# Kernel tuning notes

Measured on AMD Instinct MI355X. Metric: run time of the kernel, lower is better.

Reference implementation:

```python
import jax, jax.numpy as jnp
import numpy as np

N = 50000      # nodes
E = 800000     # edges (avg degree 16)
DIM = 256      # in_channels == heads * out_channels
H = 8          # heads
C = DIM // H   # per-head out_channels = 32
EDGE_DIM = 2
NEG_SLOPE = 0.2


def setup_inputs() -> dict:
    key = jax.random.key(0)
    ks = jax.random.split(key, 8)
    x = jax.random.normal(ks[0], (N, DIM), dtype=jnp.float32)
    edge_index = jax.random.randint(ks[1], (2, E), 0, N, dtype=jnp.int32)
    edge_attr = jax.random.normal(ks[2], (E, EDGE_DIM), dtype=jnp.float32)
    s = 1.0 / np.sqrt(DIM)
    W_l = jax.random.normal(ks[3], (DIM, H * C), dtype=jnp.float32) * s   # lin_l (src)
    W_r = jax.random.normal(ks[4], (DIM, H * C), dtype=jnp.float32) * s   # lin_r (dst)
    W_e = jax.random.normal(ks[5], (EDGE_DIM, H * C), dtype=jnp.float32) * (1.0 / np.sqrt(EDGE_DIM))
    att = jax.random.normal(ks[6], (H, C), dtype=jnp.float32) * s         # attention vector a
    bias = jnp.zeros((H * C,), dtype=jnp.float32)
    return {"x": x, "edge_index": edge_index, "edge_attr": edge_attr,
            "W_l": W_l, "W_r": W_r, "W_e": W_e, "att": att, "bias": bias}


def reference(x, edge_index, edge_attr, W_l, W_r, W_e, att, bias):
    src, dst = edge_index[0], edge_index[1]
    # --- add self loops; fill_value='mean' => scatter-mean of incoming edge_attr per node ---
    attr_sum = jax.ops.segment_sum(edge_attr, dst, num_segments=N)          # [N, 2]
    cnt = jax.ops.segment_sum(jnp.ones((edge_attr.shape[0], 1), edge_attr.dtype), dst, num_segments=N)
    loop_attr = attr_sum / jnp.maximum(cnt, 1.0)                             # [N, 2], 0 for isolated nodes
    idx = jnp.arange(N, dtype=src.dtype)
    src_a = jnp.concatenate([src, idx])                                      # [E+N]
    dst_a = jnp.concatenate([dst, idx])
    ea = jnp.concatenate([edge_attr, loop_attr], axis=0)                     # [E+N, 2]
    # --- GATv2: project src/dst/edge features ---
    x_l = (x @ W_l).reshape(N, H, C)
    x_r = (x @ W_r).reshape(N, H, C)
    e_e = (ea @ W_e).reshape(-1, H, C)                                       # [E+N, H, C]
    m = x_l[src_a] + x_r[dst_a] + e_e                                        # [E+N, H, C]
    score = jnp.einsum('ehc,hc->eh', jax.nn.leaky_relu(m, NEG_SLOPE), att)   # [E+N, H]
    # --- segment softmax over incoming edges of each dst (self loop guarantees >=1 edge) ---
    smax = jax.ops.segment_max(score, dst_a, num_segments=N)                 # [N, H]
    ex = jnp.exp(score - smax[dst_a])
    denom = jax.ops.segment_sum(ex, dst_a, num_segments=N)                   # [N, H]
    alpha = ex / denom[dst_a]                                                # [E+N, H]
    # --- weighted scatter-add of src messages ---
    out = jax.ops.segment_sum(alpha[..., None] * x_l[src_a], dst_a, num_segments=N)  # [N, H, C]
    return out.reshape(N, H * C) + bias
```

## Files before the change

kernel.cpp:

```cpp
#include <hip/hip_runtime.h>
#include <hip/hip_bf16.h>

#define NN 50000
#define NPAD 53248
#define EE 800000
#define DIM 256
#define NEG_SLOPE 0.2f
#define LOG2E 1.44269504088896f

#define GEMM_BLOCKS 1564
#define FILL_BLOCKS 3125
#define CNT_BLOCKS  3125
#define CVT_BLOCKS  12500
#define WT_BLOCKS   512

typedef __attribute__((ext_vector_type(8))) short short8;
typedef __attribute__((ext_vector_type(4))) float f32x4;
typedef __attribute__((ext_vector_type(2))) float v2f;

__device__ __forceinline__ unsigned short f2bf(float f) {
    unsigned u = __float_as_uint(f);
    unsigned r = (u + 0x7fffu + ((u >> 16) & 1u)) >> 16;
    return (unsigned short)r;
}
__device__ __forceinline__ float bf2f(unsigned short h) {
    return __uint_as_float(((unsigned)h) << 16);
}
__device__ __forceinline__ float u2f_lo(unsigned u) {
    return __uint_as_float(u << 16);
}
__device__ __forceinline__ float u2f_hi(unsigned u) {
    return __uint_as_float(u & 0xffff0000u);
}

__device__ __forceinline__ float red8(float s) {
    int t;
    t = __builtin_amdgcn_update_dpp(0, __float_as_int(s), 0xB1, 0xF, 0xF, true);
    s += __int_as_float(t);
    t = __builtin_amdgcn_update_dpp(0, __float_as_int(s), 0x4E, 0xF, 0xF, true);
    s += __int_as_float(t);
    t = __builtin_amdgcn_update_dpp(0, __float_as_int(s), 0x141, 0xF, 0xF, true);
    s += __int_as_float(t);
    return s;
}

__global__ __launch_bounds__(256) void k_prep_count(
    const float* __restrict__ x, const float* __restrict__ Wl,
    const float* __restrict__ Wr, const int* __restrict__ ei,
    unsigned short* __restrict__ xb, unsigned short* __restrict__ wt,
    int* __restrict__ cnt, int* __restrict__ rank)
{
    int b = blockIdx.x;
    if (b < CNT_BLOCKS) {
        int e = b * 256 + threadIdx.x;
        if (e < EE) {
            int dst = ei[EE + e];
            rank[e] = atomicAdd(&cnt[dst], 1);
        }
    } else if (b < CNT_BLOCKS + CVT_BLOCKS) {
        int i = ((b - CNT_BLOCKS) * 256 + threadIdx.x) * 4;
        float4 v = *(const float4*)(x + i);
        ushort4 o;
        o.x = f2bf(v.x); o.y = f2bf(v.y); o.z = f2bf(v.z); o.w = f2bf(v.w);
        *(ushort4*)(xb + i) = o;
    } else {
        int idx = (b - CNT_BLOCKS - CVT_BLOCKS) * 256 + threadIdx.x;
        int n = idx >> 8, k = idx & 255;
        float v = (n < 256) ? Wl[k * 256 + n] : Wr[k * 256 + (n - 256)];
        wt[idx] = f2bf(v);
    }
}

__global__ __launch_bounds__(1024) void k_scan(
    const int* __restrict__ cnt, int* __restrict__ row_start)
{
    __shared__ int wsum[16];
    int tid = threadIdx.x, lane = tid & 63, wid = tid >> 6;
    int4 v[13];
#pragma unroll
    for (int p = 0; p < 13; ++p)
        v[p] = *(const int4*)(cnt + p * 4096 + tid * 4);
    int carry = 0;
#pragma unroll
    for (int p = 0; p < 13; ++p) {
        int4 vv = v[p];
        int tsum = vv.x + vv.y + vv.z + vv.w;
        int s = tsum;
#pragma unroll
        for (int off = 1; off < 64; off <<= 1) {
            int t = __shfl_up(s, off, 64);
            if (lane >= off) s += t;
        }
        if (lane == 63) wsum[wid] = s;
        __syncthreads();
        int wpre = 0, tot = 0;
#pragma unroll
        for (int w = 0; w < 16; ++w) {
            int xv = wsum[w];
            tot += xv;
            if (w < wid) wpre += xv;
        }
        int ex = carry + wpre + (s - tsum);
        int4 o;
        o.x = ex;
        o.y = o.x + vv.x;
        o.z = o.y + vv.y;
        o.w = o.z + vv.z;
        *(int4*)(row_start + p * 4096 + tid * 4) = o;
        carry += tot;
        __syncthreads();
    }
}

__global__ __launch_bounds__(256) void k_gemm_fill(
    const unsigned short* __restrict__ xb, const unsigned short* __restrict__ wt,
    const int* __restrict__ ei, const float* __restrict__ ea,
    const int* __restrict__ row_start, const int* __restrict__ rank,
    unsigned short* __restrict__ xl, unsigned short* __restrict__ xr,
    uint2* __restrict__ edge_rec)
{
    __shared__ short sAB[8192];
    int tid = threadIdx.x;

    if (blockIdx.x >= GEMM_BLOCKS) {
        int e = (blockIdx.x - GEMM_BLOCKS) * 256 + tid;
        if (e < EE) {
            int src = ei[e];
            int dst = ei[EE + e];
            float2 a = *(const float2*)(ea + 2 * e);
            int pos = row_start[dst] + rank[e];
            unsigned packed = ((unsigned)f2bf(a.y) << 16) | f2bf(a.x);
            edge_rec[pos] = make_uint2((unsigned)src, packed);
        }
        return;
    }

    int bid = blockIdx.x;
    const int q = GEMM_BLOCKS / 8, r = GEMM_BLOCKS % 8;
    int xcd = bid & 7, kk = bid >> 3;
    int wg = (xcd < r) ? xcd * (q + 1) + kk
                       : r * (q + 1) + (xcd - r) * q + kk;

    int wid = tid >> 6, lane = tid & 63;
    int mt = wg >> 2, nt = wg & 3;
    int mBase = mt * 128, nBase = nt * 128;
    int wm = (wid & 1) * 64, wn = (wid >> 1) * 64;
    int qq4 = lane >> 4, mh = lane & 15;

    f32x4 acc[4][4];
#pragma unroll
    for (int i = 0; i < 4; ++i)
#pragma unroll
        for (int j = 0; j < 4; ++j)
            acc[i][j] = (f32x4){0.f, 0.f, 0.f, 0.f};

    int aoff[4], boff[4];
#pragma unroll
    for (int f = 0; f < 4; ++f) {
        int rr = wm + f * 16 + mh;
        aoff[f] = (rr * 4 + (qq4 ^ (rr & 3))) * 8;
        int nl = wn + f * 16 + mh;
        boff[f] = 4096 + (nl * 4 + (qq4 ^ (nl & 3))) * 8;
    }

    for (int k0 = 0; k0 < 256; k0 += 32) {
        __syncthreads();
#pragma unroll
        for (int it = 0; it < 4; ++it) {
            int L = it * 256 + tid;
            const unsigned short* g;
            if (L < 512) {
                int rr = L >> 2;
                int q2 = (L & 3) ^ (rr & 3);
                int grow = mBase + rr;
                if (grow > NN - 1) grow = NN - 1;
                g = xb + (size_t)grow * 256 + k0 + q2 * 8;
            } else {
                int LB = L - 512;
                int nl = LB >> 2;
                int q2 = (LB & 3) ^ (nl & 3);
                g = wt + (size_t)(nBase + nl) * 256 + k0 + q2 * 8;
            }
            short* lp = sAB + (it * 256 + wid * 64) * 8;
            __builtin_amdgcn_global_load_lds(
                (const __attribute__((address_space(1))) void*)g,
                (__attribute__((address_space(3))) void*)lp, 16, 0, 0);
        }
        __syncthreads();

        short8 af[4], bfr[4];
#pragma unroll
        for (int f = 0; f < 4; ++f) af[f]  = *(const short8*)(sAB + aoff[f]);
#pragma unroll
        for (int f = 0; f < 4; ++f) bfr[f] = *(const short8*)(sAB + boff[f]);
#pragma unroll
        for (int i = 0; i < 4; ++i)
#pragma unroll
            for (int j = 0; j < 4; ++j)
                acc[i][j] = __builtin_amdgcn_mfma_f32_16x16x32_bf16(
                    af[i], bfr[j], acc[i][j], 0, 0, 0);
    }

    unsigned short* cb = (nt < 2) ? xl : xr;
    int chalf = (nt & 1) * 128;
#pragma unroll
    for (int i = 0; i < 4; ++i)
#pragma unroll
        for (int j = 0; j < 4; ++j)
#pragma unroll
            for (int rr = 0; rr < 4; ++rr) {
                int row = mBase + wm + i * 16 + qq4 * 4 + rr;
                if (row < NN) {
                    int col = chalf + wn + j * 16 + mh;
                    cb[(size_t)row * 256 + col] = f2bf(acc[i][j][rr]);
                }
            }
}

__global__ __launch_bounds__(256) void k_attn(
    const unsigned short* __restrict__ xl, const unsigned short* __restrict__ xr,
    const int* __restrict__ row_start, const uint2* __restrict__ edge_rec,
    const float* __restrict__ W_e, const float* __restrict__ att,
    const float* __restrict__ bias, float* __restrict__ out)
{
    int n = __builtin_amdgcn_readfirstlane(blockIdx.x * 4 + (threadIdx.x >> 6));
    if (n >= NN) return;
    int lane = threadIdx.x & 63;
    int j = lane * 4;

    uint2 xru = *(const uint2*)(xr + ((size_t)n << 8) + j);
    v2f xr01 = {u2f_lo(xru.x), u2f_hi(xru.x)};
    v2f xr23 = {u2f_lo(xru.y), u2f_hi(xru.y)};
    float4 av = *(const float4*)(att + j);
    v2f att01 = {av.x * LOG2E, av.y * LOG2E};
    v2f att23 = {av.z * LOG2E, av.w * LOG2E};
    float4 w0v = *(const float4*)(W_e + j);
    float4 w1v = *(const float4*)(W_e + 256 + j);
    v2f we0_01 = {w0v.x, w0v.y}, we0_23 = {w0v.z, w0v.w};
    v2f we1_01 = {w1v.x, w1v.y}, we1_23 = {w1v.z, w1v.w};
    const v2f sl2 = {NEG_SLOPE, NEG_SLOPE};

    int rs = __builtin_amdgcn_readfirstlane(row_start[n]);
    int cn = __builtin_amdgcn_readfirstlane(row_start[n + 1]) - rs;

    float D = 0.0f, la0 = 0.0f, la1 = 0.0f;
    v2f acc01 = {0.f, 0.f}, acc23 = {0.f, 0.f};

    auto body = [&](uint2 ru, float a0, float a1) {
        v2f xl01 = {u2f_lo(ru.x), u2f_hi(ru.x)};
        v2f xl23 = {u2f_lo(ru.y), u2f_hi(ru.y)};
        v2f a0v = {a0, a0}, a1v = {a1, a1};
        v2f m01 = xl01 + xr01;
        v2f m23 = xl23 + xr23;
        m01 = __builtin_elementwise_fma(a0v, we0_01, m01);
        m23 = __builtin_elementwise_fma(a0v, we0_23, m23);
        m01 = __builtin_elementwise_fma(a1v, we1_01, m01);
        m23 = __builtin_elementwise_fma(a1v, we1_23, m23);
        v2f t01 = __builtin_elementwise_max(m01, m01 * sl2);
        v2f t23 = __builtin_elementwise_max(m23, m23 * sl2);
        v2f sv = t01 * att01;
        sv = __builtin_elementwise_fma(t23, att23, sv);
        float s = sv.x + sv.y;
        s = red8(s);
        float w = __builtin_amdgcn_exp2f(s);
        D += w;
        v2f wv = {w, w};
        acc01 = __builtin_elementwise_fma(wv, xl01, acc01);
        acc23 = __builtin_elementwise_fma(wv, xl23, acc23);
    };

    int done = 0;
    while (done < cn) {
        int m = cn - done; if (m > 64) m = 64;
        int ridx = rs + done + lane;
        if (ridx > EE + 63) ridx = EE + 63;
        uint2 rc = edge_rec[ridx];
        int rcx = (int)rc.x, rca = (int)rc.y;

        auto gat = [&](int k) -> uint2 {
            unsigned sidx = (unsigned)__builtin_amdgcn_readlane(rcx, k);
            return *(const uint2*)(xl + ((size_t)sidx << 8) + j);
        };
        auto proc = [&](uint2 xu, int k) {
            unsigned pk = (unsigned)__builtin_amdgcn_readlane(rca, k);
            float a0 = __uint_as_float(pk << 16);
            float a1 = __uint_as_float(pk & 0xffff0000u);
            la0 += a0; la1 += a1;
            body(xu, a0, a1);
        };

        uint2 x0 = gat(0), x1 = gat(1), x2 = gat(2), x3 = gat(3);
        for (int i = 0; i < m; i += 4) {
            proc(x0, i);
            if (i + 4 < m) x0 = gat(i + 4);
            if (i + 1 < m) { proc(x1, i + 1); if (i + 5 < m) x1 = gat(i + 5); }
            if (i + 2 < m) { proc(x2, i + 2); if (i + 6 < m) x2 = gat(i + 6); }
            if (i + 3 < m) { proc(x3, i + 3); if (i + 7 < m) x3 = gat(i + 7); }
        }
        done += m;
    }

    float invc = 1.0f / fmaxf((float)cn, 1.0f);
    uint2 xs = *(const uint2*)(xl + ((size_t)n << 8) + j);
    body(xs, la0 * invc, la1 * invc);

    float invD = 1.0f / D;
    float4 b4 = *(const float4*)(bias + j);
    float4 o;
    o.x = fmaf(acc01.x, invD, b4.x);
    o.y = fmaf(acc01.y, invD, b4.y);
    o.z = fmaf(acc23.x, invD, b4.z);
    o.w = fmaf(acc23.y, invD, b4.w);
    *(float4*)(out + (size_t)n * 256 + j) = o;
}

extern "C" void kernel_launch(void* const* d_in, const int* in_sizes, int n_in,
                              void* d_out, int out_size, void* d_ws, size_t ws_size,
                              hipStream_t stream)
{
    const float* x    = (const float*)d_in[0];
    const int*   ei   = (const int*)  d_in[1];
    const float* ea   = (const float*)d_in[2];
    const float* Wl   = (const float*)d_in[3];
    const float* Wr   = (const float*)d_in[4];
    const float* We   = (const float*)d_in[5];
    const float* att  = (const float*)d_in[6];
    const float* bias = (const float*)d_in[7];
    float* out = (float*)d_out;

    char* ws = (char*)d_ws;
    size_t off = 0;
    unsigned short* xl = (unsigned short*)(ws + off); off += (size_t)NN * 256 * 2;
    unsigned short* xr = (unsigned short*)(ws + off); off += (size_t)NN * 256 * 2;
    unsigned short* xb = (unsigned short*)(ws + off); off += (size_t)NN * 256 * 2;
    uint2*  edge_rec   = (uint2*)(ws + off);          off += (size_t)(EE + 64) * 8;
    int*    cnt        = (int*)(ws + off);            off += (size_t)NPAD * 4;
    int*    row_st     = (int*)(ws + off);            off += (size_t)NPAD * 4;
    int*    rank       = (int*)(ws + off);            off += (size_t)EE * 4;
    unsigned short* wt = (unsigned short*)(ws + off); off += (size_t)512 * 256 * 2;

    hipMemsetAsync(edge_rec + EE, 0, 64 * sizeof(uint2) + NPAD * sizeof(int), stream);

    k_prep_count<<<CNT_BLOCKS + CVT_BLOCKS + WT_BLOCKS, 256, 0, stream>>>(
        x, Wl, Wr, ei, xb, wt, cnt, rank);
    k_scan      <<<1, 1024, 0, stream>>>(cnt, row_st);
    k_gemm_fill <<<GEMM_BLOCKS + FILL_BLOCKS, 256, 0, stream>>>(
        xb, wt, ei, ea, row_st, rank, xl, xr, edge_rec);
    k_attn      <<<12500, 256, 0, stream>>>(
        xl, xr, row_st, edge_rec, We, att, bias, out);
}
```

Before: 268.9 us.

## Split edge counting across prep and GEMM kernels, stage GEMM output via LDS

Edge degree counting is split in half: the first half runs in the prep kernel and the second half runs as extra blocks inside the GEMM kernel. The scan and the CSR fill then move after the GEMM into separate kernels, so the GEMM is no longer waiting on the serial single-block scan. The GEMM epilogue now stages its bf16 tile through padded LDS and writes it with coalesced 16-byte stores instead of scattered 2-byte stores. This adds one kernel launch and a serialized fill kernel.

```diff
diff --git a/kernel.cpp b/kernel.cpp
--- a/kernel.cpp
+++ b/kernel.cpp
@@ -4,13 +4,15 @@
 #define NN 50000
 #define NPAD 53248
 #define EE 800000
+#define EHALF 400128
 #define DIM 256
 #define NEG_SLOPE 0.2f
 #define LOG2E 1.44269504088896f
 
 #define GEMM_BLOCKS 1564
+#define CNTA_BLOCKS 1563
+#define CNTB_BLOCKS 1562
 #define FILL_BLOCKS 3125
-#define CNT_BLOCKS  3125
 #define CVT_BLOCKS  12500
 #define WT_BLOCKS   512
 
@@ -22,9 +24,6 @@
     unsigned u = __float_as_uint(f);
     unsigned r = (u + 0x7fffu + ((u >> 16) & 1u)) >> 16;
     return (unsigned short)r;
-}
-__device__ __forceinline__ float bf2f(unsigned short h) {
-    return __uint_as_float(((unsigned)h) << 16);
 }
 __device__ __forceinline__ float u2f_lo(unsigned u) {
     return __uint_as_float(u << 16);
@@ -44,94 +43,43 @@
     return s;
 }
 
-__global__ __launch_bounds__(256) void k_prep_count(
+__global__ __launch_bounds__(256) void k_prep(
     const float* __restrict__ x, const float* __restrict__ Wl,
     const float* __restrict__ Wr, const int* __restrict__ ei,
     unsigned short* __restrict__ xb, unsigned short* __restrict__ wt,
     int* __restrict__ cnt, int* __restrict__ rank)
 {
     int b = blockIdx.x;
-    if (b < CNT_BLOCKS) {
+    if (b < CNTA_BLOCKS) {
         int e = b * 256 + threadIdx.x;
-        if (e < EE) {
-            int dst = ei[EE + e];
-            rank[e] = atomicAdd(&cnt[dst], 1);
-        }
-    } else if (b < CNT_BLOCKS + CVT_BLOCKS) {
-        int i = ((b - CNT_BLOCKS) * 256 + threadIdx.x) * 4;
+        int dst = ei[EE + e];
+        rank[e] = atomicAdd(&cnt[dst], 1);
+    } else if (b < CNTA_BLOCKS + CVT_BLOCKS) {
+        int i = ((b - CNTA_BLOCKS) * 256 + threadIdx.x) * 4;
         float4 v = *(const float4*)(x + i);
         ushort4 o;
         o.x = f2bf(v.x); o.y = f2bf(v.y); o.z = f2bf(v.z); o.w = f2bf(v.w);
         *(ushort4*)(xb + i) = o;
     } else {
-        int idx = (b - CNT_BLOCKS - CVT_BLOCKS) * 256 + threadIdx.x;
+        int idx = (b - CNTA_BLOCKS - CVT_BLOCKS) * 256 + threadIdx.x;
         int n = idx >> 8, k = idx & 255;
         float v = (n < 256) ? Wl[k * 256 + n] : Wr[k * 256 + (n - 256)];
         wt[idx] = f2bf(v);
     }
 }
 
-__global__ __launch_bounds__(1024) void k_scan(
-    const int* __restrict__ cnt, int* __restrict__ row_start)
-{
-    __shared__ int wsum[16];
-    int tid = threadIdx.x, lane = tid & 63, wid = tid >> 6;
-    int4 v[13];
-#pragma unroll
-    for (int p = 0; p < 13; ++p)
-        v[p] = *(const int4*)(cnt + p * 4096 + tid * 4);
-    int carry = 0;
-#pragma unroll
-    for (int p = 0; p < 13; ++p) {
-        int4 vv = v[p];
-        int tsum = vv.x + vv.y + vv.z + vv.w;
-        int s = tsum;
-#pragma unroll
-        for (int off = 1; off < 64; off <<= 1) {
-            int t = __shfl_up(s, off, 64);
-            if (lane >= off) s += t;
-        }
-        if (lane == 63) wsum[wid] = s;
-        __syncthreads();
-        int wpre = 0, tot = 0;
-#pragma unroll
-        for (int w = 0; w < 16; ++w) {
-            int xv = wsum[w];
-            tot += xv;
-            if (w < wid) wpre += xv;
-        }
-        int ex = carry + wpre + (s - tsum);
-        int4 o;
-        o.x = ex;
-        o.y = o.x + vv.x;
-        o.z = o.y + vv.y;
-        o.w = o.z + vv.z;
-        *(int4*)(row_start + p * 4096 + tid * 4) = o;
-        carry += tot;
-        __syncthreads();
-    }
-}
-
-__global__ __launch_bounds__(256) void k_gemm_fill(
+__global__ __launch_bounds__(256) void k_cnt_gemm(
     const unsigned short* __restrict__ xb, const unsigned short* __restrict__ wt,
-    const int* __restrict__ ei, const float* __restrict__ ea,
-    const int* __restrict__ row_start, const int* __restrict__ rank,
-    unsigned short* __restrict__ xl, unsigned short* __restrict__ xr,
-    uint2* __restrict__ edge_rec)
-{
-    __shared__ short sAB[8192];
+    const int* __restrict__ ei, int* __restrict__ cnt, int* __restrict__ rank,
+    unsigned short* __restrict__ xl, unsigned short* __restrict__ xr)
+{
+    __shared__ short sAB[8704];
     int tid = threadIdx.x;
 
     if (blockIdx.x >= GEMM_BLOCKS) {
-        int e = (blockIdx.x - GEMM_BLOCKS) * 256 + tid;
-        if (e < EE) {
-            int src = ei[e];
-            int dst = ei[EE + e];
-            float2 a = *(const float2*)(ea + 2 * e);
-            int pos = row_start[dst] + rank[e];
-            unsigned packed = ((unsigned)f2bf(a.y) << 16) | f2bf(a.x);
-            edge_rec[pos] = make_uint2((unsigned)src, packed);
-        }
+        int e = EHALF + (blockIdx.x - GEMM_BLOCKS) * 256 + tid;
+        int dst = ei[EE + e];
+        rank[e] = atomicAdd(&cnt[dst], 1);
         return;
     }
 
@@ -204,17 +152,91 @@
     unsigned short* cb = (nt < 2) ? xl : xr;
     int chalf = (nt & 1) * 128;
 #pragma unroll
-    for (int i = 0; i < 4; ++i)
-#pragma unroll
-        for (int j = 0; j < 4; ++j)
-#pragma unroll
-            for (int rr = 0; rr < 4; ++rr) {
-                int row = mBase + wm + i * 16 + qq4 * 4 + rr;
-                if (row < NN) {
-                    int col = chalf + wn + j * 16 + mh;
-                    cb[(size_t)row * 256 + col] = f2bf(acc[i][j][rr]);
-                }
-            }
+    for (int t = 0; t < 2; ++t) {
+        __syncthreads();
+        if ((wid & 1) == t) {
+#pragma unroll
+            for (int i = 0; i < 4; ++i)
+#pragma unroll
+                for (int j = 0; j < 4; ++j)
+#pragma unroll
+                    for (int rr = 0; rr < 4; ++rr) {
+                        int lrow = i * 16 + qq4 * 4 + rr;
+                        int lcol = wn + j * 16 + mh;
+                        sAB[lrow * 136 + lcol] = (short)f2bf(acc[i][j][rr]);
+                    }
+        }
+        __syncthreads();
+        int row = tid >> 2, seg = tid & 3;
+        int grow = mBase + t * 64 + row;
+        if (grow < NN) {
+            const short* lp = sAB + row * 136 + seg * 32;
+            short8 v0 = *(const short8*)(lp);
+            short8 v1 = *(const short8*)(lp + 8);
+            short8 v2 = *(const short8*)(lp + 16);
+            short8 v3 = *(const short8*)(lp + 24);
+            unsigned short* gp = cb + (size_t)grow * 256 + chalf + seg * 32;
+            *(short8*)(gp)      = v0;
+            *(short8*)(gp + 8)  = v1;
+            *(short8*)(gp + 16) = v2;
+            *(short8*)(gp + 24) = v3;
+        }
+    }
+}
+
+__global__ __launch_bounds__(1024) void k_scan(
+    const int* __restrict__ cnt, int* __restrict__ row_start)
+{
+    __shared__ int wsum[16];
+    int tid = threadIdx.x, lane = tid & 63, wid = tid >> 6;
+    int4 v[13];
+#pragma unroll
+    for (int p = 0; p < 13; ++p)
+        v[p] = *(const int4*)(cnt + p * 4096 + tid * 4);
+    int carry = 0;
+#pragma unroll
+    for (int p = 0; p < 13; ++p) {
+        int4 vv = v[p];
+        int tsum = vv.x + vv.y + vv.z + vv.w;
+        int s = tsum;
+#pragma unroll
+        for (int off = 1; off < 64; off <<= 1) {
+            int t = __shfl_up(s, off, 64);
+            if (lane >= off) s += t;
+        }
+        if (lane == 63) wsum[wid] = s;
+        __syncthreads();
+        int wpre = 0, tot = 0;
+#pragma unroll
+        for (int w = 0; w < 16; ++w) {
+            int xv = wsum[w];
+            tot += xv;
+            if (w < wid) wpre += xv;
+        }
+        int ex = carry + wpre + (s - tsum);
+        int4 o;
+        o.x = ex;
+        o.y = o.x + vv.x;
+        o.z = o.y + vv.y;
+        o.w = o.z + vv.z;
+        *(int4*)(row_start + p * 4096 + tid * 4) = o;
+        carry += tot;
+        __syncthreads();
+    }
+}
+
+__global__ __launch_bounds__(256) void k_fill(
+    const int* __restrict__ ei, const float* __restrict__ ea,
+    const int* __restrict__ row_start, const int* __restrict__ rank,
+    uint2* __restrict__ edge_rec)
+{
+    int e = blockIdx.x * 256 + threadIdx.x;
+    int src = ei[e];
+    int dst = ei[EE + e];
+    float2 a = *(const float2*)(ea + 2 * e);
+    int pos = row_start[dst] + rank[e];
+    unsigned packed = ((unsigned)f2bf(a.y) << 16) | f2bf(a.x);
+    edge_rec[pos] = make_uint2((unsigned)src, packed);
 }
 
 __global__ __launch_bounds__(256) void k_attn(
@@ -341,11 +363,13 @@
 
     hipMemsetAsync(edge_rec + EE, 0, 64 * sizeof(uint2) + NPAD * sizeof(int), stream);
 
-    k_prep_count<<<CNT_BLOCKS + CVT_BLOCKS + WT_BLOCKS, 256, 0, stream>>>(
+    k_prep    <<<CNTA_BLOCKS + CVT_BLOCKS + WT_BLOCKS, 256, 0, stream>>>(
         x, Wl, Wr, ei, xb, wt, cnt, rank);
-    k_scan      <<<1, 1024, 0, stream>>>(cnt, row_st);
-    k_gemm_fill <<<GEMM_BLOCKS + FILL_BLOCKS, 256, 0, stream>>>(
-        xb, wt, ei, ea, row_st, rank, xl, xr, edge_rec);
-    k_attn      <<<12500, 256, 0, stream>>>(
+    k_cnt_gemm<<<GEMM_BLOCKS + CNTB_BLOCKS, 256, 0, stream>>>(
+        xb, wt, ei, cnt, rank, xl, xr);
+    k_scan    <<<1, 1024, 0, stream>>>(cnt, row_st);
+    k_fill    <<<FILL_BLOCKS, 256, 0, stream>>>(
+        ei, ea, row_st, rank, edge_rec);
+    k_attn    <<<12500, 256, 0, stream>>>(
         xl, xr, row_st, edge_rec, We, att, bias, out);
 }
```

Result: slower. 299.2 us (+11.3%).
